# Optimization experiments

Hardware: AMD Instinct MI355X
Metric: run time of the kernel (lower is better)

Reference implementation:

```python
import jax, jax.numpy as jnp
import numpy as np

K_NEIGHBORS = 16
N_CLASSES = 10


def setup_inputs() -> dict:
    key = jax.random.key(0)
    k1, k2, k3 = jax.random.split(key, 3)
    x = jax.random.normal(k1, (2048, 128), dtype=jnp.float32)
    train_data = jax.random.normal(k2, (100000, 128), dtype=jnp.float32)
    train_labels = jax.random.randint(k3, (100000,), 0, N_CLASSES, dtype=jnp.int64)
    return {"x": x, "train_data": train_data, "train_labels": train_labels}


def reference(x, train_data, train_labels):
    N = x.shape[0]
    x2 = jnp.sum(x * x, axis=1, keepdims=True)            # [N, 1]
    t2 = jnp.sum(train_data * train_data, axis=1)          # [M]
    d2 = x2 + t2[None, :] - 2.0 * (x @ train_data.T)       # [N, M]
    dist = jnp.sqrt(jnp.maximum(d2, 0.0))
    # smallest-k via top_k on negated distances
    neg_d, idx = jax.lax.top_k(-dist, K_NEIGHBORS)         # [N, K]
    d = -neg_d
    labels = train_labels[idx]                              # [N, K]
    # weights == 'distance': inverse distance; rows containing an exact match
    # (inf weight) get a 0/1 indicator vector instead.
    w = 1.0 / d
    inf_mask = jnp.isinf(w)
    inf_row = jnp.any(inf_mask, axis=1, keepdims=True)
    w = jnp.where(inf_row, inf_mask.astype(jnp.float32), w)
    # weighted vote: scatter-add weights into per-class buckets
    rows = jnp.arange(N)[:, None]
    proba = jnp.zeros((N, N_CLASSES), jnp.float32).at[rows, labels].add(w)
    s = jnp.sum(proba, axis=1, keepdims=True)
    s = jnp.where(s == 0.0, 1.0, s)
    proba = proba / s
    pred = jnp.argmax(proba, axis=1)
    return pred, proba
```

## Files before the change

### kernel.cpp

```cpp
#include <hip/hip_runtime.h>
#include <hip/hip_fp16.h>
#include <math.h>

#define M_TRAIN 100000
#define NQ 2048
#define DIM 128
#define KNN 16
#define NCLS 10

#define S_STRIDE 16
#define S_CNT (M_TRAIN / S_STRIDE)
#define S_PAD 6272
#define SCH 49
#define SPC 128
#define TT 64
#define MQ 128
#define QSTR 136

#define CAP 768
#define TBH 50176
#define NTR 128
#define NQT 64
#define MARGIN 3.0f
#define SLACK 7.0f

using bfrag = __attribute__((ext_vector_type(8))) short;
using cfrag = __attribute__((ext_vector_type(4))) float;

__device__ __forceinline__ bool better(float d1, int i1, float d2, int i2) {
    return (d1 < d2) || (d1 == d2 && i1 < i2);
}

__device__ __forceinline__ unsigned pack_bf16(float a, float b) {
    unsigned ua = __float_as_uint(a), ub = __float_as_uint(b);
    ua += 0x7fffu + ((ua >> 16) & 1u);
    ub += 0x7fffu + ((ub >> 16) & 1u);
    return (ua >> 16) | (ub & 0xffff0000u);
}

__device__ __forceinline__ void gload_lds16(const void* g, void* l) {
    __builtin_amdgcn_global_load_lds(
        (const __attribute__((address_space(1))) unsigned int*)g,
        (__attribute__((address_space(3))) unsigned int*)l, 16, 0, 0);
}

__global__ void knn_norms(const float* __restrict__ train,
                          const float* __restrict__ x,
                          float* __restrict__ t2, float* __restrict__ x2,
                          int* __restrict__ cnt) {
    int gid = blockIdx.x * blockDim.x + threadIdx.x;
    if (gid < NQ) cnt[gid] = 0;
    int gw = gid >> 6;
    int lane = threadIdx.x & 63;
    if (gw >= M_TRAIN + NQ) return;
    const float* r = (gw < M_TRAIN) ? (train + (size_t)gw * DIM)
                                    : (x + (size_t)(gw - M_TRAIN) * DIM);
    float a = r[lane];
    float b = r[lane + 64];
    float s = a * a + b * b;
    #pragma unroll
    for (int off = 32; off > 0; off >>= 1)
        s += __shfl_down(s, off, 64);
    if (lane == 0) {
        if (gw < M_TRAIN) t2[gw] = s; else x2[gw - M_TRAIN] = s;
    }
}

__global__ __launch_bounds__(256, 2)
void knn_sub_mfma(const float* __restrict__ x, const float* __restrict__ train,
                  const float* __restrict__ t2, const float* __restrict__ x2,
                  __half* __restrict__ dsub) {
    __shared__ short Q[MQ * QSTR];
    __shared__ short T[TT * QSTR];
    __shared__ float t2h[TT];
    int tid = threadIdx.x;
    int w = tid >> 6, lane = tid & 63;
    int rquad = lane >> 4, rcol = lane & 15;
    int qBase = blockIdx.y * MQ;
    int cBase = blockIdx.x * SPC;

    #pragma unroll
    for (int it = 0; it < 16; ++it) {
        int f = it * 256 + tid;
        int row = f >> 5, c4 = f & 31;
        float4 v = ((const float4*)x)[(size_t)(qBase + row) * (DIM / 4) + c4];
        uint2 p; p.x = pack_bf16(v.x, v.y); p.y = pack_bf16(v.z, v.w);
        *(uint2*)&Q[row * QSTR + c4 * 4] = p;
    }
    __syncthreads();

    float x2r[2][4];
    #pragma unroll
    for (int rt = 0; rt < 2; ++rt)
        #pragma unroll
        for (int reg = 0; reg < 4; ++reg)
            x2r[rt][reg] = x2[qBase + w * 32 + rt * 16 + rquad * 4 + reg];

    bfrag A[2][4];
    #pragma unroll
    for (int rt = 0; rt < 2; ++rt)
        #pragma unroll
        for (int ks = 0; ks < 4; ++ks) {
            int r = w * 32 + rt * 16 + rcol;
            A[rt][ks] = *(const bfrag*)&Q[r * QSTR + ks * 32 + rquad * 8];
        }

    const cfrag zero4 = {0.f, 0.f, 0.f, 0.f};
    for (int t = 0; t < 2; ++t) {
        __syncthreads();
        int sBase = cBase + t * TT;
        #pragma unroll
        for (int it = 0; it < 8; ++it) {
            int f = it * 256 + tid;
            int row = f >> 5, c4 = f & 31;
            int sj = sBase + row;
            bool ok = sj < S_CNT;
            float4 v = ok ? ((const float4*)train)[(size_t)sj * S_STRIDE * (DIM / 4) + c4]
                          : make_float4(0.f, 0.f, 0.f, 0.f);
            uint2 p; p.x = pack_bf16(v.x, v.y); p.y = pack_bf16(v.z, v.w);
            *(uint2*)&T[row * QSTR + c4 * 4] = p;
        }
        if (tid < TT) {
            int sj = sBase + tid;
            t2h[tid] = (sj < S_CNT) ? t2[(size_t)sj * S_STRIDE] : 1e30f;
        }
        __syncthreads();

        cfrag acc[2][4];
        #pragma unroll
        for (int ks = 0; ks < 4; ++ks) {
            bfrag B[4];
            #pragma unroll
            for (int ct = 0; ct < 4; ++ct) {
                int n = ct * 16 + rcol;
                B[ct] = *(const bfrag*)&T[n * QSTR + ks * 32 + rquad * 8];
            }
            #pragma unroll
            for (int rt = 0; rt < 2; ++rt)
                #pragma unroll
                for (int ct = 0; ct < 4; ++ct)
                    acc[rt][ct] = (ks == 0)
                        ? __builtin_amdgcn_mfma_f32_16x16x32_bf16(A[rt][0], B[ct], zero4, 0, 0, 0)
                        : __builtin_amdgcn_mfma_f32_16x16x32_bf16(A[rt][ks], B[ct], acc[rt][ct], 0, 0, 0);
        }

        float th[4];
        #pragma unroll
        for (int ct = 0; ct < 4; ++ct) th[ct] = t2h[ct * 16 + rcol];
        #pragma unroll
        for (int rt = 0; rt < 2; ++rt)
            #pragma unroll
            for (int ct = 0; ct < 4; ++ct)
                #pragma unroll
                for (int reg = 0; reg < 4; ++reg) {
                    float d2 = x2r[rt][reg] + th[ct] - 2.f * acc[rt][ct][reg];
                    int qrow = qBase + w * 32 + rt * 16 + rquad * 4 + reg;
                    int col = sBase + ct * 16 + rcol;
                    dsub[(size_t)qrow * S_PAD + col] = __float2half_rn(d2);
                }
    }
}

__global__ __launch_bounds__(256)
void knn_select(const __half* __restrict__ dsub, float* __restrict__ tau) {
    __shared__ float wv[4];
    __shared__ int   wc[4];
    __shared__ float sv;
    __shared__ int   sc;
    int q = blockIdx.x, tid = threadIdx.x;
    int w = tid >> 6, lane = tid & 63;

    float bd[KNN];
    #pragma unroll
    for (int j = 0; j < KNN; ++j) bd[j] = 3.4e38f;
    for (int k = 0; k < 25; ++k) {
        int idx = k * 256 + tid;
        if (idx < S_PAD) {
            float v = __half2float(dsub[(size_t)q * S_PAD + idx]);
            if (v < bd[KNN - 1]) {
                bd[KNN - 1] = v;
                #pragma unroll
                for (int j = KNN - 1; j >= 1; --j)
                    if (bd[j] < bd[j - 1]) { float t = bd[j]; bd[j] = bd[j - 1]; bd[j - 1] = t; }
            }
        }
    }

    float last = 3.4e38f;
    for (int sel = 0; sel < KNN; ++sel) {
        float mv = bd[0]; int mj = 0;
        #pragma unroll
        for (int j = 1; j < KNN; ++j) if (bd[j] < mv) { mv = bd[j]; mj = j; }
        int mc = (tid << 4) | mj;
        #pragma unroll
        for (int off = 32; off > 0; off >>= 1) {
            float ov = __shfl_down(mv, off, 64);
            int   oc = __shfl_down(mc, off, 64);
            if (ov < mv) { mv = ov; mc = oc; }
        }
        if (lane == 0) { wv[w] = mv; wc[w] = mc; }
        __syncthreads();
        if (tid == 0) {
            float bv = wv[0]; int bc = wc[0];
            #pragma unroll
            for (int i = 1; i < 4; ++i) if (wv[i] < bv) { bv = wv[i]; bc = wc[i]; }
            sv = bv; sc = bc;
        }
        __syncthreads();
        last = sv;
        if (tid == (sc >> 4)) {
            int j0 = sc & 15;
            #pragma unroll
            for (int j = 0; j < KNN; ++j) if (j == j0) bd[j] = 3.4e38f;
        }
        __syncthreads();
    }
    if (tid == 0) tau[q] = last;
}

__global__ __launch_bounds__(256)
void knn_convert_bf16(const float* __restrict__ train,
                      unsigned int* __restrict__ tb, int rowBase,
                      const float* __restrict__ x,
                      unsigned int* __restrict__ xb) {
    int b = blockIdx.x;
    if (b >= (TBH * 32) / 256) {
        int i = (b - (TBH * 32) / 256) * 256 + threadIdx.x;
        int row = i >> 5, seg = i & 31;
        float4 v = ((const float4*)x)[(size_t)row * (DIM / 4) + seg];
        uint2 p; p.x = pack_bf16(v.x, v.y); p.y = pack_bf16(v.z, v.w);
        ((uint2*)xb)[(size_t)row * 32 + seg] = p;
        return;
    }
    int i = b * 256 + threadIdx.x;
    int row = i >> 5, seg = i & 31;
    int g = rowBase + row;
    float4 v = (g < M_TRAIN)
        ? ((const float4*)train)[(size_t)g * (DIM / 4) + seg]
        : make_float4(0.f, 0.f, 0.f, 0.f);
    uint2 p; p.x = pack_bf16(v.x, v.y); p.y = pack_bf16(v.z, v.w);
    int off = (seg * 8) ^ ((row & 7) << 4);
    *(uint2*)((char*)tb + (size_t)row * 256 + off) = p;
}

__global__ __launch_bounds__(256, 4)
void knn_filter8(const unsigned int* __restrict__ xbb,
                 const short* __restrict__ tbb,
                 const float* __restrict__ t2, const float* __restrict__ x2,
                 const float* __restrict__ tau, int pBase0,
                 int* __restrict__ buf_i, unsigned short* __restrict__ buf_h,
                 int* __restrict__ cnt) {
    __shared__ __align__(16) short T[NTR * DIM];
    int tid = threadIdx.x;
    int w = tid >> 6, lane = tid & 63;
    int rquad = lane >> 4, rcol = lane & 15;

    int bid = blockIdx.x;
    int xcd = bid & 7, r = bid >> 3;
    int qb = r & 31;
    int nch = xcd + 8 * (r >> 5);
    int qBase = qb * NQT;
    int tbase = pBase0 + nch * NTR;

    const char* gsrc = (const char*)tbb + (size_t)nch * NTR * 256 + w * 8192 + lane * 16;
    char* ldst = (char*)T + w * 8192;
    #pragma unroll
    for (int i = 0; i < 8; ++i)
        gload_lds16(gsrc + i * 1024, ldst + i * 1024);

    bfrag A[4];
    int qrow = qBase + w * 16 + rcol;
    const char* xrow = (const char*)xbb + (size_t)qrow * 256;
    #pragma unroll
    for (int ks = 0; ks < 4; ++ks)
        A[ks] = *(const bfrag*)(xrow + ks * 64 + rquad * 16);

    float RC[4], x2q[4];
    #pragma unroll
    for (int reg = 0; reg < 4; ++reg) {
        int q = qBase + w * 16 + rquad * 4 + reg;
        x2q[reg] = x2[q];
        RC[reg] = 0.5f * (x2q[reg] - tau[q] - MARGIN);
    }
    float th[8];
    #pragma unroll
    for (int ct = 0; ct < 8; ++ct)
        th[ct] = 0.5f * t2[tbase + ct * 16 + rcol];
    __syncthreads();

    int swz = (rcol & 7) << 4;
    int cs[4];
    #pragma unroll
    for (int ks = 0; ks < 4; ++ks)
        cs[ks] = (ks * 64 + rquad * 16) ^ swz;

    const cfrag zero4 = {0.f, 0.f, 0.f, 0.f};
    cfrag acc[8];
    #pragma unroll
    for (int ks = 0; ks < 4; ++ks)
        #pragma unroll
        for (int ct = 0; ct < 8; ++ct) {
            const bfrag B = *(const bfrag*)((const char*)T + (ct * 16 + rcol) * 256 + cs[ks]);
            acc[ct] = (ks == 0)
                ? __builtin_amdgcn_mfma_f32_16x16x32_bf16(A[0], B, zero4, 0, 0, 0)
                : __builtin_amdgcn_mfma_f32_16x16x32_bf16(A[ks], B, acc[ct], 0, 0, 0);
        }

    __syncthreads();
    __half*   d2l = (__half*)T;
    unsigned* pw  = (unsigned*)((char*)T + 16384);

    bool okidx = (tbase + 112 + rcol) < M_TRAIN;
    unsigned passw = 0;
    #pragma unroll
    for (int ct = 0; ct < 8; ++ct) {
        int idx = tbase + ct * 16 + rcol;
        bool ok = idx < M_TRAIN;
        float t2f = 2.f * th[ct];
        #pragma unroll
        for (int reg = 0; reg < 4; ++reg) {
            bool pass = ok && (acc[ct][reg] >= RC[reg] + th[ct]);
            if (pass) {
                passw |= 1u << (ct * 4 + reg);
                float d2a = x2q[reg] + t2f - 2.f * acc[ct][reg];
                d2l[(w * 16 + rquad * 4 + reg) * 128 + ct * 16 + rcol] =
                    __float2half_rn(d2a);
            }
        }
    }
    (void)okidx;
    pw[tid] = passw;
    __syncthreads();

    if (tid < 64) {
        int ww = tid >> 4, rq = (tid >> 2) & 3, rg = tid & 3;
        const unsigned* pwr = pw + ww * 64 + rq * 16;
        unsigned em[16];
        int cntq = 0;
        #pragma unroll
        for (int c = 0; c < 16; ++c) {
            unsigned e = (pwr[c] >> rg) & 0x11111111u;
            em[c] = e;
            cntq += __popc(e);
        }
        int q = qBase + tid;
        int slot = atomicAdd(&cnt[q], cntq);
        const unsigned short* d2s = (const unsigned short*)T;
        #pragma unroll
        for (int c = 0; c < 16; ++c) {
            unsigned e = em[c];
            while (e) {
                int b = __builtin_ctz(e); e &= e - 1;
                int idxl = (b >> 2) * 16 + c;
                if (slot < CAP) {
                    buf_i[(size_t)q * CAP + slot] = tbase + idxl;
                    buf_h[(size_t)q * CAP + slot] = d2s[tid * 128 + idxl];
                }
                ++slot;
            }
        }
    }
}

__global__ __launch_bounds__(256)
void knn_final(const float* __restrict__ x,
               const float* __restrict__ train,
               const float* __restrict__ t2v,
               const float* __restrict__ x2v,
               const int* __restrict__ buf_i,
               const __half* __restrict__ buf_h,
               const int* __restrict__ cnt,
               const int* __restrict__ labels,
               float* __restrict__ out) {
    __shared__ float sd[CAP];
    __shared__ int   si[CAP];
    __shared__ int   keep[CAP];
    __shared__ float wk[64];
    __shared__ int   kr[KNN];
    __shared__ float sthr;
    __shared__ int   smcnt;
    int q = blockIdx.x;
    int tid = threadIdx.x;
    int w = tid >> 6, lane = tid & 63;
    int grp = lane >> 4, sub = lane & 15;
    int n = cnt[q]; if (n > CAP) n = CAP;
    if (tid == 0) smcnt = 0;
    if (tid < KNN) kr[tid] = -1;

    float av[3];
    #pragma unroll
    for (int j = 0; j < 3; ++j) {
        int i = (w * 3 + j) * 64 + lane;
        av[j] = (i < n) ? __half2float(buf_h[(size_t)q * CAP + i]) : 3.4e38f;
    }
    for (int sel = 0; sel < KNN; ++sel) {
        float mv = av[0]; int mc = (lane << 2);
        if (av[1] < mv) { mv = av[1]; mc = (lane << 2) | 1; }
        if (av[2] < mv) { mv = av[2]; mc = (lane << 2) | 2; }
        #pragma unroll
        for (int off = 32; off > 0; off >>= 1) {
            float ov = __shfl_down(mv, off, 64);
            int   oc = __shfl_down(mc, off, 64);
            if (ov < mv || (ov == mv && oc < mc)) { mv = ov; mc = oc; }
        }
        mv = __shfl(mv, 0, 64);
        mc = __shfl(mc, 0, 64);
        if (lane == 0) wk[w * KNN + sel] = mv;
        if (lane == (mc >> 2)) {
            int j0 = mc & 3;
            if (j0 == 0) av[0] = 3.4e38f;
            else if (j0 == 1) av[1] = 3.4e38f;
            else av[2] = 3.4e38f;
        }
    }
    __syncthreads();
    if (tid < 64) {
        float v = wk[tid];
        int rank = 0;
        #pragma unroll 8
        for (int j = 0; j < 64; ++j) {
            float u = wk[j];
            if (u < v || (u == v && j < tid)) ++rank;
        }
        if (rank == KNN - 1) sthr = v + SLACK;
    }
    __syncthreads();
    float thr = sthr;

    for (int i = tid; i < n; i += 256) {
        float h = __half2float(buf_h[(size_t)q * CAP + i]);
        if (h <= thr) {
            int p = atomicAdd(&smcnt, 1);
            keep[p] = buf_i[(size_t)q * CAP + i];
        }
    }
    __syncthreads();
    int m = smcnt;

    const float4* xq = (const float4*)&x[(size_t)q * DIM + sub * 8];
    float4 qa = xq[0], qb = xq[1];
    float x2l = x2v[q];
    for (int base = 0; base < m; base += 16) {
        int i = base + w * 4 + grp;
        if (i < m) {
            int idx = keep[i];
            const float4* tr = (const float4*)&train[(size_t)idx * DIM + sub * 8];
            float4 ta = tr[0], tb4 = tr[1];
            float s = qa.x * ta.x + qa.y * ta.y + qa.z * ta.z + qa.w * ta.w
                    + qb.x * tb4.x + qb.y * tb4.y + qb.z * tb4.z + qb.w * tb4.w;
            s += __shfl_xor(s, 1, 64);
            s += __shfl_xor(s, 2, 64);
            s += __shfl_xor(s, 4, 64);
            s += __shfl_xor(s, 8, 64);
            if (sub == 0) { sd[i] = x2l + t2v[idx] - 2.f * s; si[i] = idx; }
        }
    }
    __syncthreads();

    for (int i = tid; i < m; i += 256) {
        float d = sd[i]; int ix = si[i];
        int rank = 0;
        for (int j = 0; j < m; ++j)
            if (better(sd[j], si[j], d, ix)) ++rank;
        if (rank < KNN) kr[rank] = i;
    }
    __syncthreads();

    if (tid == 0) {
        bool anyzero = false;
        float dist[KNN]; int kidx[KNN];
        #pragma unroll
        for (int j = 0; j < KNN; ++j) {
            int ii = kr[j];
            if (ii >= 0) {
                dist[j] = sqrtf(fmaxf(sd[ii], 0.f));
                kidx[j] = si[ii];
                if (dist[j] == 0.f) anyzero = true;
            } else { dist[j] = -1.f; kidx[j] = -1; }
        }
        float spr[NCLS];
        #pragma unroll
        for (int c = 0; c < NCLS; ++c) spr[c] = 0.f;
        #pragma unroll
        for (int j = 0; j < KNN; ++j) {
            int idxj = kidx[j];
            if (idxj < 0 || idxj >= M_TRAIN) continue;
            float wgt = anyzero ? (dist[j] == 0.f ? 1.f : 0.f) : 1.f / dist[j];
            spr[labels[idxj]] += wgt;
        }
        float s = 0.f;
        #pragma unroll
        for (int c = 0; c < NCLS; ++c) s += spr[c];
        if (s == 0.f) s = 1.f;
        float inv = 1.f / s;
        float best = -1.f; int bc = 0;
        #pragma unroll
        for (int c = 0; c < NCLS; ++c) {
            float pv = spr[c] * inv;
            out[NQ + (size_t)q * NCLS + c] = pv;
            if (pv > best) { best = pv; bc = c; }
        }
        out[q] = (float)bc;
    }
}

extern "C" void kernel_launch(void* const* d_in, const int* in_sizes, int n_in,
                              void* d_out, int out_size, void* d_ws, size_t ws_size,
                              hipStream_t stream) {
    const float* x      = (const float*)d_in[0];
    const float* train  = (const float*)d_in[1];
    const int*   labels = (const int*)d_in[2];
    float* out = (float*)d_out;

    char* base = (char*)d_ws;
    float*  t2   = (float*)(base);
    float*  x2   = (float*)(base + 401408);
    float*  tau  = (float*)(base + 409600);
    int*    cnt  = (int*)  (base + 417792);
    char*   region = base + 425984;
    __half* dsub = (__half*)region;
    unsigned int* tb = (unsigned int*)region;
    int*    bi   = (int*)(region + 12845056);
    unsigned int* xb = (unsigned int*)(region + 19136512);
    __half* bh   = (__half*)(region + 19660800);

    int nrows = M_TRAIN + NQ;
    knn_norms<<<(nrows * 64 + 255) / 256, 256, 0, stream>>>(train, x, t2, x2, cnt);

    dim3 gs(SCH, NQ / MQ);
    knn_sub_mfma<<<gs, 256, 0, stream>>>(x, train, t2, x2, dsub);

    knn_select<<<NQ, 256, 0, stream>>>(dsub, tau);

    for (int h = 0; h < 2; ++h) {
        int rowBase = h * TBH;
        int cgrid = (TBH * 32) / 256 + (h == 0 ? (NQ * 32) / 256 : 0);
        knn_convert_bf16<<<cgrid, 256, 0, stream>>>(train, tb, rowBase, x, xb);
        knn_filter8<<<(TBH / NTR) * (NQ / NQT), 256, 0, stream>>>(
            xb, (const short*)tb, t2, x2, tau, rowBase, bi, (unsigned short*)bh, cnt);
    }

    knn_final<<<NQ, 256, 0, stream>>>(x, train, t2, x2, bi, bh, cnt, labels, out);
}
```

Measured before the change: 414.8 us.

## Restructure filter so each wave owns its train rows and compacts via ballot

The filter kernel now gives each wave its own 32 training rows against all 64 queries of the tile, so each wave reads only its own LDS region. That lets the block-wide barriers become a per-wave vmcnt wait. Survivor compaction moves from a serial loop in a single wave (going through LDS bitmasks) to ballot plus popcount prefix offsets, with every lane writing its own candidate directly. The trade-off is more global atomics on the per-query counters, since each wave now reserves slots separately, and more A-fragment registers per lane.

```diff
diff --git a/kernel.cpp b/kernel.cpp
--- a/kernel.cpp
+++ b/kernel.cpp
@@ -244,12 +244,12 @@
 }
 
 __global__ __launch_bounds__(256, 4)
-void knn_filter8(const unsigned int* __restrict__ xbb,
-                 const short* __restrict__ tbb,
-                 const float* __restrict__ t2, const float* __restrict__ x2,
-                 const float* __restrict__ tau, int pBase0,
-                 int* __restrict__ buf_i, unsigned short* __restrict__ buf_h,
-                 int* __restrict__ cnt) {
+void knn_filter10(const unsigned int* __restrict__ xbb,
+                  const short* __restrict__ tbb,
+                  const float* __restrict__ t2, const float* __restrict__ x2,
+                  const float* __restrict__ tau, int pBase0,
+                  int* __restrict__ buf_i, unsigned short* __restrict__ buf_h,
+                  int* __restrict__ cnt) {
     __shared__ __align__(16) short T[NTR * DIM];
     int tid = threadIdx.x;
     int w = tid >> 6, lane = tid & 63;
@@ -268,98 +268,103 @@
     for (int i = 0; i < 8; ++i)
         gload_lds16(gsrc + i * 1024, ldst + i * 1024);
 
-    bfrag A[4];
-    int qrow = qBase + w * 16 + rcol;
-    const char* xrow = (const char*)xbb + (size_t)qrow * 256;
+    bfrag A[4][4];
+    #pragma unroll
+    for (int qt = 0; qt < 4; ++qt) {
+        const char* xrow = (const char*)xbb + (size_t)(qBase + qt * 16 + rcol) * 256;
+        #pragma unroll
+        for (int ks = 0; ks < 4; ++ks)
+            A[qt][ks] = *(const bfrag*)(xrow + ks * 64 + rquad * 16);
+    }
+    int row0 = tbase + w * 32 + rcol;
+    float th0 = 0.5f * t2[row0];
+    float th1 = 0.5f * t2[row0 + 16];
+
+    asm volatile("s_waitcnt vmcnt(0)" ::: "memory");
+    __builtin_amdgcn_sched_barrier(0);
+
+    int swz = (rcol & 7) << 4;
+    const char* Tw = (const char*)T + w * 8192 + rcol * 256;
+
+    const cfrag zero4 = {0.f, 0.f, 0.f, 0.f};
+    cfrag acc[4][2];
     #pragma unroll
     for (int ks = 0; ks < 4; ++ks)
-        A[ks] = *(const bfrag*)(xrow + ks * 64 + rquad * 16);
-
-    float RC[4], x2q[4];
-    #pragma unroll
-    for (int reg = 0; reg < 4; ++reg) {
-        int q = qBase + w * 16 + rquad * 4 + reg;
-        x2q[reg] = x2[q];
-        RC[reg] = 0.5f * (x2q[reg] - tau[q] - MARGIN);
-    }
-    float th[8];
-    #pragma unroll
-    for (int ct = 0; ct < 8; ++ct)
-        th[ct] = 0.5f * t2[tbase + ct * 16 + rcol];
-    __syncthreads();
-
-    int swz = (rcol & 7) << 4;
-    int cs[4];
-    #pragma unroll
-    for (int ks = 0; ks < 4; ++ks)
-        cs[ks] = (ks * 64 + rquad * 16) ^ swz;
-
-    const cfrag zero4 = {0.f, 0.f, 0.f, 0.f};
-    cfrag acc[8];
-    #pragma unroll
-    for (int ks = 0; ks < 4; ++ks)
-        #pragma unroll
-        for (int ct = 0; ct < 8; ++ct) {
-            const bfrag B = *(const bfrag*)((const char*)T + (ct * 16 + rcol) * 256 + cs[ks]);
-            acc[ct] = (ks == 0)
-                ? __builtin_amdgcn_mfma_f32_16x16x32_bf16(A[0], B, zero4, 0, 0, 0)
-                : __builtin_amdgcn_mfma_f32_16x16x32_bf16(A[ks], B, acc[ct], 0, 0, 0);
-        }
-
-    __syncthreads();
-    __half*   d2l = (__half*)T;
-    unsigned* pw  = (unsigned*)((char*)T + 16384);
-
-    bool okidx = (tbase + 112 + rcol) < M_TRAIN;
-    unsigned passw = 0;
-    #pragma unroll
-    for (int ct = 0; ct < 8; ++ct) {
-        int idx = tbase + ct * 16 + rcol;
-        bool ok = idx < M_TRAIN;
-        float t2f = 2.f * th[ct];
+        #pragma unroll
+        for (int ctl = 0; ctl < 2; ++ctl) {
+            const bfrag B = *(const bfrag*)(Tw + ctl * 4096 + ((ks * 64 + rquad * 16) ^ swz));
+            #pragma unroll
+            for (int qt = 0; qt < 4; ++qt)
+                acc[qt][ctl] = (ks == 0)
+                    ? __builtin_amdgcn_mfma_f32_16x16x32_bf16(A[qt][0], B, zero4, 0, 0, 0)
+                    : __builtin_amdgcn_mfma_f32_16x16x32_bf16(A[qt][ks], B, acc[qt][ctl], 0, 0, 0);
+        }
+
+    float x2s[4][4], tqs[4][4];
+    #pragma unroll
+    for (int qt = 0; qt < 4; ++qt) {
+        int q0 = qBase + qt * 16 + rquad * 4;
+        float4 xv = *(const float4*)&x2[q0];
+        float4 tv = *(const float4*)&tau[q0];
+        x2s[qt][0] = xv.x; x2s[qt][1] = xv.y; x2s[qt][2] = xv.z; x2s[qt][3] = xv.w;
+        tqs[qt][0] = tv.x; tqs[qt][1] = tv.y; tqs[qt][2] = tv.z; tqs[qt][3] = tv.w;
+    }
+
+    bool ok0 = row0 < M_TRAIN;
+    bool ok1 = (row0 + 16) < M_TRAIN;
+    unsigned gm[4][4];
+    #pragma unroll
+    for (int qt = 0; qt < 4; ++qt)
         #pragma unroll
         for (int reg = 0; reg < 4; ++reg) {
-            bool pass = ok && (acc[ct][reg] >= RC[reg] + th[ct]);
-            if (pass) {
-                passw |= 1u << (ct * 4 + reg);
-                float d2a = x2q[reg] + t2f - 2.f * acc[ct][reg];
-                d2l[(w * 16 + rquad * 4 + reg) * 128 + ct * 16 + rcol] =
-                    __float2half_rn(d2a);
+            float rc = 0.5f * (x2s[qt][reg] - tqs[qt][reg] - MARGIN);
+            bool p0 = ok0 && (acc[qt][0][reg] >= rc + th0);
+            bool p1 = ok1 && (acc[qt][1][reg] >= rc + th1);
+            unsigned long long m0 = __ballot(p0);
+            unsigned long long m1 = __ballot(p1);
+            unsigned g0 = (unsigned)(m0 >> (rquad * 16)) & 0xFFFFu;
+            unsigned g1 = (unsigned)(m1 >> (rquad * 16)) & 0xFFFFu;
+            gm[qt][reg] = g0 | (g1 << 16);
+        }
+
+    int baseR[4][4];
+    #pragma unroll
+    for (int qt = 0; qt < 4; ++qt)
+        #pragma unroll
+        for (int reg = 0; reg < 4; ++reg)
+            if (rcol == 0)
+                baseR[qt][reg] = atomicAdd(&cnt[qBase + qt * 16 + rquad * 4 + reg],
+                                           __popc(gm[qt][reg]));
+
+    int lsrc = lane & 48;
+    unsigned lb = 1u << rcol;
+    #pragma unroll
+    for (int qt = 0; qt < 4; ++qt)
+        #pragma unroll
+        for (int reg = 0; reg < 4; ++reg) {
+            int b = __shfl(baseR[qt][reg], lsrc, 64);
+            unsigned g = gm[qt][reg];
+            unsigned g0 = g & 0xFFFFu, g1 = g >> 16;
+            int q = qBase + qt * 16 + rquad * 4 + reg;
+            if (g0 & lb) {
+                int slot = b + __popc(g0 & (lb - 1));
+                if (slot < CAP) {
+                    buf_i[(size_t)q * CAP + slot] = row0;
+                    float d2a = x2s[qt][reg] + 2.f * th0 - 2.f * acc[qt][0][reg];
+                    buf_h[(size_t)q * CAP + slot] =
+                        __half_as_ushort(__float2half_rn(d2a));
+                }
             }
-        }
-    }
-    (void)okidx;
-    pw[tid] = passw;
-    __syncthreads();
-
-    if (tid < 64) {
-        int ww = tid >> 4, rq = (tid >> 2) & 3, rg = tid & 3;
-        const unsigned* pwr = pw + ww * 64 + rq * 16;
-        unsigned em[16];
-        int cntq = 0;
-        #pragma unroll
-        for (int c = 0; c < 16; ++c) {
-            unsigned e = (pwr[c] >> rg) & 0x11111111u;
-            em[c] = e;
-            cntq += __popc(e);
-        }
-        int q = qBase + tid;
-        int slot = atomicAdd(&cnt[q], cntq);
-        const unsigned short* d2s = (const unsigned short*)T;
-        #pragma unroll
-        for (int c = 0; c < 16; ++c) {
-            unsigned e = em[c];
-            while (e) {
-                int b = __builtin_ctz(e); e &= e - 1;
-                int idxl = (b >> 2) * 16 + c;
+            if (g1 & lb) {
+                int slot = b + __popc(g0) + __popc(g1 & (lb - 1));
                 if (slot < CAP) {
-                    buf_i[(size_t)q * CAP + slot] = tbase + idxl;
-                    buf_h[(size_t)q * CAP + slot] = d2s[tid * 128 + idxl];
+                    buf_i[(size_t)q * CAP + slot] = row0 + 16;
+                    float d2a = x2s[qt][reg] + 2.f * th1 - 2.f * acc[qt][1][reg];
+                    buf_h[(size_t)q * CAP + slot] =
+                        __half_as_ushort(__float2half_rn(d2a));
                 }
-                ++slot;
             }
         }
-    }
 }
 
 __global__ __launch_bounds__(256)
@@ -536,7 +541,7 @@
         int rowBase = h * TBH;
         int cgrid = (TBH * 32) / 256 + (h == 0 ? (NQ * 32) / 256 : 0);
         knn_convert_bf16<<<cgrid, 256, 0, stream>>>(train, tb, rowBase, x, xb);
-        knn_filter8<<<(TBH / NTR) * (NQ / NQT), 256, 0, stream>>>(
+        knn_filter10<<<(TBH / NTR) * (NQ / NQT), 256, 0, stream>>>(
             xb, (const short*)tb, t2, x2, tau, rowBase, bi, (unsigned short*)bh, cnt);
     }
 
```

Result: slower. 549.4 us (+32.5%).
